# Optimization experiments

Measured on AMD Instinct MI355X. Metric: run time of the kernel, lower is better.

## Reference

```python
import jax, jax.numpy as jnp
import numpy as np

B, S, D = 1, 2048, 2048          # batch, context_length, embedding_dimension
H, DH = 16, 128                  # num_heads, head_size (= head_output_dimension)
HID = 4 * D                      # SwiGLU hidden dim
LAMBDA_INIT = 0.8
EPS = 1e-6


def setup_inputs() -> dict:
    key = jax.random.key(0)
    ks = jax.random.split(key, 14)
    nrm = lambda k, sh, s=0.02: jax.random.normal(k, sh, jnp.float32) * s
    return {
        "x": jax.random.normal(ks[0], (B, S, D), jnp.float32),
        "g_norm": jnp.ones((D,), jnp.float32),          # shared RMSNorm gain (same layer used twice)
        "Wq1": nrm(ks[1], (H, D, DH)), "Wq2": nrm(ks[2], (H, D, DH)),
        "Wk1": nrm(ks[3], (H, D, DH)), "Wk2": nrm(ks[4], (H, D, DH)),
        "Wv":  nrm(ks[5], (H, D, DH)),
        "lq1": nrm(ks[6], (H, DH), 0.1), "lk1": nrm(ks[7], (H, DH), 0.1),
        "lq2": nrm(ks[8], (H, DH), 0.1), "lk2": nrm(ks[9], (H, DH), 0.1),
        "Wo": nrm(ks[10], (H * DH, D)),
        "W1": nrm(ks[11], (D, HID)), "W2": nrm(ks[12], (D, HID)), "W3": nrm(ks[13], (HID, D)),
    }


def rmsnorm(x, g):
    return x * jax.lax.rsqrt(jnp.mean(x * x, axis=-1, keepdims=True) + EPS) * g


def diff_attention(x, Wq1, Wq2, Wk1, Wk2, Wv, lq1, lk1, lq2, lk2, Wo):
    # per-head projections: [B,S,D] x [H,D,DH] -> [B,H,S,DH]
    proj = lambda W: jnp.einsum('bsd,hde->bhse', x, W)
    q1, q2 = proj(Wq1), proj(Wq2)
    k1, k2 = proj(Wk1), proj(Wk2)
    v = proj(Wv)
    scale = 1.0 / jnp.sqrt(jnp.float32(DH))
    A1 = jax.nn.softmax(jnp.einsum('bhse,bhte->bhst', q1, k1) * scale, axis=-1)
    A2 = jax.nn.softmax(jnp.einsum('bhse,bhte->bhst', q2, k2) * scale, axis=-1)
    # learned per-head lambda: exp(lq1.lk1) - exp(lq2.lk2) + lambda_init
    lam = (jnp.exp(jnp.sum(lq1 * lk1, -1)) - jnp.exp(jnp.sum(lq2 * lk2, -1)) + LAMBDA_INIT)  # [H]
    o = jnp.einsum('bhst,bhte->bhse', A1 - lam[None, :, None, None] * A2, v)  # [B,H,S,DH]
    o = o.transpose(0, 2, 1, 3).reshape(B, S, H * DH)
    return o @ Wo


def reference(x, g_norm, Wq1, Wq2, Wk1, Wk2, Wv, lq1, lk1, lq2, lk2, Wo, W1, W2, W3):
    # Encoder block (dropout=0 -> identity in eval)
    h = rmsnorm(x, g_norm)
    h = diff_attention(h, Wq1, Wq2, Wk1, Wk2, Wv, lq1, lk1, lq2, lk2, Wo) + h
    z = rmsnorm(h, g_norm)
    ffn = (jax.nn.silu(z @ W1) * (z @ W2)) @ W3  # SwiGLU
    return ffn + h
```

## Files before the change

### kernel.cpp

```cpp
#include <hip/hip_runtime.h>

typedef unsigned short u16;
typedef __bf16 bf16x8 __attribute__((ext_vector_type(8)));
typedef float f32x4 __attribute__((ext_vector_type(4)));

#define S_LEN 2048
#define D_DIM 2048
#define NH 16
#define DH 128
#define HID 8192

__device__ __forceinline__ u16 f2bf(float f) {
  unsigned int u = __float_as_uint(f);
  u += 0x7fff + ((u >> 16) & 1);
  return (u16)(u >> 16);
}

__device__ __forceinline__ void gld16(const u16* g, u16* l) {
  __builtin_amdgcn_global_load_lds(
      (const __attribute__((address_space(1))) unsigned int*)g,
      (__attribute__((address_space(3))) unsigned int*)l, 16, 0, 0);
}

__global__ __launch_bounds__(256) void tconv_f2b(const float* __restrict__ in,
                                                 u16* __restrict__ out, int R, int C) {
  __shared__ float tile[32][33];
  size_t boff = (size_t)blockIdx.z * R * C;
  in += boff; out += boff;
  int c0 = blockIdx.x * 32, r0 = blockIdx.y * 32;
  int tx = threadIdx.x, ty = threadIdx.y;
#pragma unroll
  for (int i = 0; i < 32; i += 8) tile[ty + i][tx] = in[(size_t)(r0 + ty + i) * C + c0 + tx];
  __syncthreads();
#pragma unroll
  for (int i = 0; i < 32; i += 8) out[(size_t)(c0 + ty + i) * R + r0 + tx] = f2bf(tile[tx][ty + i]);
}

__global__ __launch_bounds__(256) void tconv_b2b(const u16* __restrict__ in,
                                                 u16* __restrict__ out, int R, int C) {
  __shared__ u16 tile[32][34];
  size_t boff = (size_t)blockIdx.z * R * C;
  in += boff; out += boff;
  int c0 = blockIdx.x * 32, r0 = blockIdx.y * 32;
  int tx = threadIdx.x, ty = threadIdx.y;
#pragma unroll
  for (int i = 0; i < 32; i += 8) tile[ty + i][tx] = in[(size_t)(r0 + ty + i) * C + c0 + tx];
  __syncthreads();
#pragma unroll
  for (int i = 0; i < 32; i += 8) out[(size_t)(c0 + ty + i) * R + r0 + tx] = tile[tx][ty + i];
}

__global__ __launch_bounds__(256) void rmsnorm_kernel(const float* __restrict__ x,
                                                      const float* __restrict__ g,
                                                      float* __restrict__ xf,
                                                      u16* __restrict__ xb) {
  int row = blockIdx.x;
  int t = threadIdx.x;
  const float4* xr = (const float4*)(x + (size_t)row * D_DIM);
  float4 v0 = xr[t];
  float4 v1 = xr[t + 256];
  float ss = v0.x * v0.x + v0.y * v0.y + v0.z * v0.z + v0.w * v0.w +
             v1.x * v1.x + v1.y * v1.y + v1.z * v1.z + v1.w * v1.w;
#pragma unroll
  for (int o = 1; o < 64; o <<= 1) ss += __shfl_xor(ss, o, 64);
  __shared__ float wss[4];
  if ((t & 63) == 0) wss[t >> 6] = ss;
  __syncthreads();
  float tot = wss[0] + wss[1] + wss[2] + wss[3];
  float rs = rsqrtf(tot * (1.0f / D_DIM) + 1e-6f);
  const float4* gr = (const float4*)g;
  float4 g0 = gr[t], g1 = gr[t + 256];
  float4 o0, o1;
  o0.x = v0.x * rs * g0.x; o0.y = v0.y * rs * g0.y; o0.z = v0.z * rs * g0.z; o0.w = v0.w * rs * g0.w;
  o1.x = v1.x * rs * g1.x; o1.y = v1.y * rs * g1.y; o1.z = v1.z * rs * g1.z; o1.w = v1.w * rs * g1.w;
  if (xf) {
    float4* xfr = (float4*)(xf + (size_t)row * D_DIM);
    xfr[t] = o0; xfr[t + 256] = o1;
  }
  ushort4 b0, b1;
  b0.x = f2bf(o0.x); b0.y = f2bf(o0.y); b0.z = f2bf(o0.z); b0.w = f2bf(o0.w);
  b1.x = f2bf(o1.x); b1.y = f2bf(o1.y); b1.z = f2bf(o1.z); b1.w = f2bf(o1.w);
  ushort4* xbr = (ushort4*)(xb + (size_t)row * D_DIM);
  xbr[t] = b0; xbr[t + 256] = b1;
}

__global__ __launch_bounds__(256) void lam_kernel(const float* __restrict__ lq1,
                                                  const float* __restrict__ lk1,
                                                  const float* __restrict__ lq2,
                                                  const float* __restrict__ lk2,
                                                  float* __restrict__ lamw) {
  int t = threadIdx.x;
  int h = t >> 4, i = (t & 15) << 3;
  float d1 = 0.f, d2 = 0.f;
#pragma unroll
  for (int j = 0; j < 8; j++) {
    d1 += lq1[h * DH + i + j] * lk1[h * DH + i + j];
    d2 += lq2[h * DH + i + j] * lk2[h * DH + i + j];
  }
#pragma unroll
  for (int o = 1; o < 16; o <<= 1) { d1 += __shfl_xor(d1, o, 64); d2 += __shfl_xor(d2, o, 64); }
  if ((t & 15) == 0) lamw[h] = __expf(d1) - __expf(d2) + 0.8f;
}

template <int MODE, int BN>
__global__ __launch_bounds__(256) void gemm_a(const u16* __restrict__ A,
                                              const u16* __restrict__ Bt,
                                              const u16* __restrict__ Bt2,
                                              void* __restrict__ Cout,
                                              const float* __restrict__ res,
                                              int M, int N, int K, long sBt, long sC) {
  constexpr int BM = 128, BK = 32;
  constexpr int JF = BN / 32;
  __shared__ __align__(16) u16 As[2][BM * BK];
  __shared__ __align__(16) u16 Bs[2][BN * BK];
  __shared__ __align__(16) u16 Bs2[(MODE == 2) ? 2 : 1][(MODE == 2) ? BN * BK : 8];
  const int t = threadIdx.x;
  const int lane = t & 63, wid = t >> 6;
  const int wm = (wid >> 1) * 64, wn = (wid & 1) * (BN / 2);
  const int fr = lane & 15, fq = lane >> 4;

  const int gx = gridDim.x, gy = gridDim.y;
  const int total = gx * gy * (int)gridDim.z;
  int flat = ((int)blockIdx.z * gy + (int)blockIdx.y) * gx + (int)blockIdx.x;
  {
    int q = total >> 3, r = total & 7;
    int xcd = flat & 7, pos = flat >> 3;
    flat = ((xcd < r) ? xcd * (q + 1) : r * (q + 1) + (xcd - r) * q) + pos;
  }
  const int bz = flat / (gx * gy);
  const int r2 = flat % (gx * gy);
  const int by = r2 / gx, bx = r2 % gx;

  const int m0 = by * BM, n0 = bx * BN;
  const u16* bt = Bt + (long)bz * sBt;
  f32x4 acc[4][JF] = {};
  f32x4 acc2[(MODE == 2) ? 4 : 1][(MODE == 2) ? JF : 1] = {};
  const int sr = t >> 2, sc = (t & 3) << 3;
  const u16* aG = A + (long)(m0 + sr) * K + sc;
  const u16* bG = bt + (long)(n0 + sr) * K + sc;
  const u16* b2G = (MODE == 2) ? (Bt2 + (long)(n0 + sr) * K + sc) : nullptr;

  auto stage = [&](int buf, int k0) {
    gld16(aG + k0, &As[buf][t * 8]);
    gld16(aG + (long)64 * K + k0, &As[buf][t * 8 + 64 * BK]);
    gld16(bG + k0, &Bs[buf][t * 8]);
    if (BN == 128) gld16(bG + (long)64 * K + k0, &Bs[buf][t * 8 + 64 * BK]);
    if (MODE == 2) {
      gld16(b2G + k0, &Bs2[buf][t * 8]);
      if (BN == 128) gld16(b2G + (long)64 * K + k0, &Bs2[buf][t * 8 + 64 * BK]);
    }
  };

  stage(0, 0);
  __syncthreads();

  int cur = 0;
  for (int k0 = 0; k0 < K; k0 += BK) {
    if (k0 + BK < K) stage(cur ^ 1, k0 + BK);

    bf16x8 af[4], bfr[JF];
#pragma unroll
    for (int i = 0; i < 4; i++) af[i] = *(const bf16x8*)&As[cur][(wm + i * 16 + fr) * BK + fq * 8];
#pragma unroll
    for (int j = 0; j < JF; j++) bfr[j] = *(const bf16x8*)&Bs[cur][(wn + j * 16 + fr) * BK + fq * 8];
    bf16x8 cf[(MODE == 2) ? JF : 1];
    if (MODE == 2) {
#pragma unroll
      for (int j = 0; j < JF; j++) cf[j] = *(const bf16x8*)&Bs2[cur][(wn + j * 16 + fr) * BK + fq * 8];
    }

    __builtin_amdgcn_s_setprio(1);
#pragma unroll
    for (int i = 0; i < 4; i++)
#pragma unroll
      for (int j = 0; j < JF; j++)
        acc[i][j] = __builtin_amdgcn_mfma_f32_16x16x32_bf16(af[i], bfr[j], acc[i][j], 0, 0, 0);
    if (MODE == 2) {
#pragma unroll
      for (int i = 0; i < 4; i++)
#pragma unroll
        for (int j = 0; j < JF; j++)
          acc2[i][j] = __builtin_amdgcn_mfma_f32_16x16x32_bf16(af[i], cf[j], acc2[i][j], 0, 0, 0);
    }
    __builtin_amdgcn_s_setprio(0);

    __syncthreads();
    cur ^= 1;
  }

#pragma unroll
  for (int i = 0; i < 4; i++)
#pragma unroll
    for (int j = 0; j < JF; j++) {
      int row0 = m0 + wm + i * 16 + (fq << 2);
      int col = n0 + wn + j * 16 + fr;
#pragma unroll
      for (int r = 0; r < 4; r++) {
        long idx = (long)(row0 + r) * N + col;
        float v = acc[i][j][r];
        if (MODE == 0) {
          ((u16*)Cout + (long)bz * sC)[idx] = f2bf(v);
        } else if (MODE == 1) {
          ((float*)Cout)[idx] = v + res[idx];
        } else {
          float g2 = acc2[i][j][r];
          float sg = v / (1.0f + __expf(-v));
          ((u16*)Cout)[idx] = f2bf(sg * g2);
        }
      }
    }
}

#define LDK 136
#define LDV 40
#define LDP 40

__global__ __launch_bounds__(256) void flash_attn(const u16* __restrict__ q1g,
                                                  const u16* __restrict__ q2g,
                                                  const u16* __restrict__ k1g,
                                                  const u16* __restrict__ k2g,
                                                  const u16* __restrict__ vtg,
                                                  const float* __restrict__ lamw,
                                                  u16* __restrict__ og) {
  __shared__ __align__(16) u16 Ks1[32 * LDK];
  __shared__ __align__(16) u16 Ks2[32 * LDK];
  __shared__ __align__(16) u16 Vs[128 * LDV];
  __shared__ __align__(16) u16 Ps[4 * 2 * 16 * LDP];
  const float scale = 0.08838834764831845f;
  int h = blockIdx.y, qt = blockIdx.x;
  size_t hoff = (size_t)h * S_LEN * DH;
  const u16* q1 = q1g + hoff;
  const u16* q2 = q2g + hoff;
  const u16* k1 = k1g + hoff;
  const u16* k2 = k2g + hoff;
  const u16* vt = vtg + hoff;
  int t = threadIdx.x, wid = t >> 6, lane = t & 63;
  int fr = lane & 15, fq = lane >> 4;
  int qrow = qt * 64 + wid * 16 + fr;
  bf16x8 qf1[4], qf2[4];
#pragma unroll
  for (int ks = 0; ks < 4; ks++) {
    qf1[ks] = *(const bf16x8*)&q1[(size_t)qrow * DH + ks * 32 + fq * 8];
    qf2[ks] = *(const bf16x8*)&q2[(size_t)qrow * DH + ks * 32 + fq * 8];
  }
  bf16x8 ones;
#pragma unroll
  for (int i = 0; i < 8; i++) ones[i] = (__bf16)1.0f;

  f32x4 O1[8] = {};
  f32x4 O2[8] = {};
  f32x4 L1 = {};
  f32x4 L2 = {};
  int skr = t >> 3, skc = (t & 7) << 4;
  int svr = t >> 2, svc = (t & 3) << 3;
  u16* myP1 = &Ps[(wid * 2 + 0) * 16 * LDP];
  u16* myP2 = &Ps[(wid * 2 + 1) * 16 * LDP];

  for (int kt = 0; kt < S_LEN; kt += 32) {
    uint4 ka1 = *(const uint4*)&k1[(size_t)(kt + skr) * DH + skc];
    uint4 kb1 = *(const uint4*)&k1[(size_t)(kt + skr) * DH + skc + 8];
    uint4 ka2 = *(const uint4*)&k2[(size_t)(kt + skr) * DH + skc];
    uint4 kb2 = *(const uint4*)&k2[(size_t)(kt + skr) * DH + skc + 8];
    uint4 va = *(const uint4*)&vt[(size_t)svr * S_LEN + kt + svc];
    uint4 vb = *(const uint4*)&vt[(size_t)(svr + 64) * S_LEN + kt + svc];
    __syncthreads();
    *(uint4*)&Ks1[skr * LDK + skc] = ka1;
    *(uint4*)&Ks1[skr * LDK + skc + 8] = kb1;
    *(uint4*)&Ks2[skr * LDK + skc] = ka2;
    *(uint4*)&Ks2[skr * LDK + skc + 8] = kb2;
    *(uint4*)&Vs[svr * LDV + svc] = va;
    *(uint4*)&Vs[(svr + 64) * LDV + svc] = vb;
    __syncthreads();

    f32x4 s1[2] = {};
    f32x4 s2[2] = {};
#pragma unroll
    for (int nf = 0; nf < 2; nf++)
#pragma unroll
      for (int ks = 0; ks < 4; ks++) {
        bf16x8 b1v = *(const bf16x8*)&Ks1[(nf * 16 + fr) * LDK + ks * 32 + fq * 8];
        s1[nf] = __builtin_amdgcn_mfma_f32_16x16x32_bf16(qf1[ks], b1v, s1[nf], 0, 0, 0);
        bf16x8 b2v = *(const bf16x8*)&Ks2[(nf * 16 + fr) * LDK + ks * 32 + fq * 8];
        s2[nf] = __builtin_amdgcn_mfma_f32_16x16x32_bf16(qf2[ks], b2v, s2[nf], 0, 0, 0);
      }

#pragma unroll
    for (int nf = 0; nf < 2; nf++)
#pragma unroll
      for (int r = 0; r < 4; r++) {
        myP1[(fq * 4 + r) * LDP + nf * 16 + fr] = f2bf(__expf(s1[nf][r] * scale));
        myP2[(fq * 4 + r) * LDP + nf * 16 + fr] = f2bf(__expf(s2[nf][r] * scale));
      }
    asm volatile("s_waitcnt lgkmcnt(0)" ::: "memory");
    bf16x8 pa1 = *(const bf16x8*)&myP1[fr * LDP + fq * 8];
    bf16x8 pa2 = *(const bf16x8*)&myP2[fr * LDP + fq * 8];
    L1 = __builtin_amdgcn_mfma_f32_16x16x32_bf16(pa1, ones, L1, 0, 0, 0);
    L2 = __builtin_amdgcn_mfma_f32_16x16x32_bf16(pa2, ones, L2, 0, 0, 0);
#pragma unroll
    for (int f = 0; f < 8; f++) {
      bf16x8 bv = *(const bf16x8*)&Vs[(f * 16 + fr) * LDV + fq * 8];
      O1[f] = __builtin_amdgcn_mfma_f32_16x16x32_bf16(pa1, bv, O1[f], 0, 0, 0);
      O2[f] = __builtin_amdgcn_mfma_f32_16x16x32_bf16(pa2, bv, O2[f], 0, 0, 0);
    }
  }

  float lam = lamw[h];
#pragma unroll
  for (int r = 0; r < 4; r++) {
    float i1 = 1.0f / L1[r], i2 = lam / L2[r];
#pragma unroll
    for (int f = 0; f < 8; f++) {
      float val = O1[f][r] * i1 - O2[f][r] * i2;
      og[(size_t)(qt * 64 + wid * 16 + fq * 4 + r) * (NH * DH) + h * DH + f * 16 + fr] =
          f2bf(val);
    }
  }
}

extern "C" void kernel_launch(void* const* d_in, const int* in_sizes, int n_in,
                              void* d_out, int out_size, void* d_ws, size_t ws_size,
                              hipStream_t stream) {
  const float* x = (const float*)d_in[0];
  const float* g = (const float*)d_in[1];
  const float* Wq1 = (const float*)d_in[2];
  const float* Wq2 = (const float*)d_in[3];
  const float* Wk1 = (const float*)d_in[4];
  const float* Wk2 = (const float*)d_in[5];
  const float* Wv = (const float*)d_in[6];
  const float* lq1 = (const float*)d_in[7];
  const float* lk1 = (const float*)d_in[8];
  const float* lq2 = (const float*)d_in[9];
  const float* lk2 = (const float*)d_in[10];
  const float* Wo = (const float*)d_in[11];
  const float* W1 = (const float*)d_in[12];
  const float* W2 = (const float*)d_in[13];
  const float* W3 = (const float*)d_in[14];

  char* ws = (char*)d_ws;
  size_t off = 0;
  auto alloc = [&](size_t b) {
    char* p = ws + off;
    off += (b + 255) & ~(size_t)255;
    return p;
  };
  const size_t PROJ_B = (size_t)NH * DH * D_DIM * 2;
  u16* wq1t = (u16*)alloc(PROJ_B);
  u16* wq2t = (u16*)alloc(PROJ_B);
  u16* wk1t = (u16*)alloc(PROJ_B);
  u16* wk2t = (u16*)alloc(PROJ_B);
  u16* wvt = (u16*)alloc(PROJ_B);
  u16* wot = (u16*)alloc((size_t)D_DIM * NH * DH * 2);
  u16* w1t = (u16*)alloc((size_t)HID * D_DIM * 2);
  u16* w2t = (u16*)alloc((size_t)HID * D_DIM * 2);
  u16* w3t = (u16*)alloc((size_t)D_DIM * HID * 2);
  u16* xnb = (u16*)alloc((size_t)S_LEN * D_DIM * 2);
  float* xnf = (float*)alloc((size_t)S_LEN * D_DIM * 4);
  u16* q1b = (u16*)alloc(PROJ_B);
  u16* q2b = (u16*)alloc(PROJ_B);
  u16* k1b = (u16*)alloc(PROJ_B);
  u16* k2b = (u16*)alloc(PROJ_B);
  u16* vb = (u16*)alloc(PROJ_B);
  u16* vtb = (u16*)alloc(PROJ_B);
  float* lamw = (float*)alloc(NH * 4);
  u16* oa = (u16*)alloc((size_t)S_LEN * NH * DH * 2);
  float* hf = (float*)alloc((size_t)S_LEN * D_DIM * 4);
  u16* zb = (u16*)alloc((size_t)S_LEN * D_DIM * 2);
  u16* ffb = (u16*)alloc((size_t)S_LEN * HID * 2);
  if (off > ws_size) return;

  dim3 tpb(32, 8);
  tconv_f2b<<<dim3(DH / 32, D_DIM / 32, NH), tpb, 0, stream>>>(Wq1, wq1t, D_DIM, DH);
  tconv_f2b<<<dim3(DH / 32, D_DIM / 32, NH), tpb, 0, stream>>>(Wq2, wq2t, D_DIM, DH);
  tconv_f2b<<<dim3(DH / 32, D_DIM / 32, NH), tpb, 0, stream>>>(Wk1, wk1t, D_DIM, DH);
  tconv_f2b<<<dim3(DH / 32, D_DIM / 32, NH), tpb, 0, stream>>>(Wk2, wk2t, D_DIM, NH == 16 ? DH : DH);
  tconv_f2b<<<dim3(DH / 32, D_DIM / 32, NH), tpb, 0, stream>>>(Wv, wvt, D_DIM, DH);
  tconv_f2b<<<dim3(D_DIM / 32, (NH * DH) / 32, 1), tpb, 0, stream>>>(Wo, wot, NH * DH, D_DIM);
  tconv_f2b<<<dim3(HID / 32, D_DIM / 32, 1), tpb, 0, stream>>>(W1, w1t, D_DIM, HID);
  tconv_f2b<<<dim3(HID / 32, D_DIM / 32, 1), tpb, 0, stream>>>(W2, w2t, D_DIM, HID);
  tconv_f2b<<<dim3(D_DIM / 32, HID / 32, 1), tpb, 0, stream>>>(W3, w3t, HID, D_DIM);

  rmsnorm_kernel<<<S_LEN, 256, 0, stream>>>(x, g, xnf, xnb);
  lam_kernel<<<1, 256, 0, stream>>>(lq1, lk1, lq2, lk2, lamw);

  long sB = (long)DH * D_DIM, sC = (long)S_LEN * DH;
  gemm_a<0, 128><<<dim3(1, S_LEN / 128, 80), 256, 0, stream>>>(
      xnb, wq1t, nullptr, q1b, nullptr, S_LEN, DH, D_DIM, sB, sC);
  tconv_b2b<<<dim3(DH / 32, S_LEN / 32, NH), tpb, 0, stream>>>(vb, vtb, S_LEN, DH);

  flash_attn<<<dim3(S_LEN / 64, NH), 256, 0, stream>>>(q1b, q2b, k1b, k2b, vtb, lamw, oa);

  gemm_a<1, 64><<<dim3(D_DIM / 64, S_LEN / 128, 1), 256, 0, stream>>>(
      oa, wot, nullptr, hf, xnf, S_LEN, D_DIM, NH * DH, 0, 0);
  rmsnorm_kernel<<<S_LEN, 256, 0, stream>>>(hf, g, nullptr, zb);
  gemm_a<2, 64><<<dim3(HID / 64, S_LEN / 128, 1), 256, 0, stream>>>(
      zb, w1t, w2t, ffb, nullptr, S_LEN, HID, D_DIM, 0, 0);
  gemm_a<1, 64><<<dim3(D_DIM / 64, S_LEN / 128, 1), 256, 0, stream>>>(
      ffb, w3t, nullptr, d_out, hf, S_LEN, D_DIM, HID, 0, 0);
}
```

Before: 978.9 us.

## Add dedicated 256x128 triple-buffered GEMM for fused QKV projections; drop XCD remap

Replaces the generic gemm_a launch for the five per-head projections with a new 512-thread kernel using 256x128x64 tiles, three-stage LDS buffering with XOR-swizzled layout, and interleaved prefetch with MFMA phases under raised priority. It treats all five projection weights as one N=10240 matrix, so outputs land in per-head layout. It also removes the XCD-aware block remapping from gemm_a, which may change L2 locality for the remaining GEMMs. The larger tile raises LDS use (about 144 KB) and register pressure, which limits occupancy.

After: 979.0 us. Within noise of the previous version (+0.0%).

```diff
diff --git a/kernel.cpp b/kernel.cpp
--- a/kernel.cpp
+++ b/kernel.cpp
@@ -100,6 +100,110 @@
 #pragma unroll
   for (int o = 1; o < 16; o <<= 1) { d1 += __shfl_xor(d1, o, 64); d2 += __shfl_xor(d2, o, 64); }
   if ((t & 15) == 0) lamw[h] = __expf(d1) - __expf(d2) + 0.8f;
+}
+
+__global__ __launch_bounds__(512) void gemm8_proj(const u16* __restrict__ A,
+                                                  const u16* __restrict__ Bt,
+                                                  u16* __restrict__ Out,
+                                                  int M, int N, int K) {
+  constexpr int BM = 256, BN = 128, BK = 64, NBUF = 3;
+  __shared__ __align__(16) u16 As[NBUF][BM * BK];
+  __shared__ __align__(16) u16 Bs[NBUF][BN * BK];
+  const int t = threadIdx.x;
+  const int lane = t & 63;
+  const int wid = t >> 6;
+  const int wm = (wid >> 2) * 128;
+  const int wn = (wid & 3) * 32;
+  const int fr = lane & 15, fq = lane >> 4;
+  const int m0 = blockIdx.y * BM, n0 = blockIdx.x * BN;
+
+  f32x4 acc[8][2] = {};
+
+  const int sro = t >> 3;
+  const int scol = ((((t & 7) ^ (sro & 7)) << 4) >> 1);
+  const u16* aSrc = A + (size_t)(m0 + sro) * K + scol;
+  const u16* bSrc = Bt + (size_t)(n0 + sro) * K + scol;
+
+  const int NT = K >> 6;
+
+#define STAGE_A(buf, k0, s) gld16(aSrc + (size_t)((s)*64) * K + (k0), &As[buf][(s)*4096 + t * 8])
+#define STAGE_B(buf, k0, s) gld16(bSrc + (size_t)((s)*64) * K + (k0), &Bs[buf][(s)*4096 + t * 8])
+
+  STAGE_A(0, 0, 0); STAGE_A(0, 0, 1); STAGE_A(0, 0, 2); STAGE_A(0, 0, 3);
+  STAGE_B(0, 0, 0); STAGE_B(0, 0, 1);
+  STAGE_A(1, BK, 0); STAGE_A(1, BK, 1); STAGE_A(1, BK, 2); STAGE_A(1, BK, 3);
+  STAGE_B(1, BK, 0); STAGE_B(1, BK, 1);
+  asm volatile("s_waitcnt vmcnt(6)" ::: "memory");
+  __builtin_amdgcn_s_barrier();
+
+  const int swz = (fr & 7) << 4;
+
+  for (int tk = 0; tk < NT; ++tk) {
+    const int r = tk % 3;
+    const int pf = tk + 2;
+    const int pbuf = pf % 3;
+    const bool doPf = pf < NT;
+    const int k0pf = pf << 6;
+
+    bf16x8 bfrag[2][2];
+#pragma unroll
+    for (int j = 0; j < 2; ++j)
+#pragma unroll
+      for (int kk = 0; kk < 2; ++kk) {
+        int row = wn + j * 16 + fr;
+        int cb = (kk * 64 + fq * 16) ^ swz;
+        bfrag[j][kk] = *(const bf16x8*)&Bs[r][row * 64 + (cb >> 1)];
+      }
+
+#pragma unroll
+    for (int ph = 0; ph < 2; ++ph) {
+      if (doPf) {
+        if (ph == 0) { STAGE_A(pbuf, k0pf, 0); STAGE_A(pbuf, k0pf, 1); STAGE_B(pbuf, k0pf, 0); }
+        else         { STAGE_A(pbuf, k0pf, 2); STAGE_A(pbuf, k0pf, 3); STAGE_B(pbuf, k0pf, 1); }
+      }
+      bf16x8 af[4][2];
+#pragma unroll
+      for (int i = 0; i < 4; ++i)
+#pragma unroll
+        for (int kk = 0; kk < 2; ++kk) {
+          int row = wm + ph * 64 + i * 16 + fr;
+          int cb = (kk * 64 + fq * 16) ^ swz;
+          af[i][kk] = *(const bf16x8*)&As[r][row * 64 + (cb >> 1)];
+        }
+      __builtin_amdgcn_s_setprio(1);
+#pragma unroll
+      for (int i = 0; i < 4; ++i)
+#pragma unroll
+        for (int j = 0; j < 2; ++j) {
+          acc[ph * 4 + i][j] =
+              __builtin_amdgcn_mfma_f32_16x16x32_bf16(af[i][0], bfrag[j][0], acc[ph * 4 + i][j], 0, 0, 0);
+          acc[ph * 4 + i][j] =
+              __builtin_amdgcn_mfma_f32_16x16x32_bf16(af[i][1], bfrag[j][1], acc[ph * 4 + i][j], 0, 0, 0);
+        }
+      __builtin_amdgcn_s_setprio(0);
+    }
+
+    if (tk + 1 < NT) {
+      if (doPf) asm volatile("s_waitcnt vmcnt(6)" ::: "memory");
+      else      asm volatile("s_waitcnt vmcnt(0)" ::: "memory");
+      __builtin_amdgcn_s_barrier();
+    }
+  }
+
+#undef STAGE_A
+#undef STAGE_B
+
+  const size_t headBase = (size_t)(n0 >> 7) * ((size_t)S_LEN * 128);
+#pragma unroll
+  for (int i = 0; i < 8; ++i)
+#pragma unroll
+    for (int j = 0; j < 2; ++j) {
+      int row0 = m0 + wm + i * 16 + (fq << 2);
+      int colL = wn + j * 16 + fr;
+#pragma unroll
+      for (int rr = 0; rr < 4; ++rr)
+        Out[headBase + (size_t)(row0 + rr) * 128 + colL] = f2bf(acc[i][j][rr]);
+    }
 }
 
 template <int MODE, int BN>
@@ -118,20 +222,8 @@
   const int lane = t & 63, wid = t >> 6;
   const int wm = (wid >> 1) * 64, wn = (wid & 1) * (BN / 2);
   const int fr = lane & 15, fq = lane >> 4;
-
-  const int gx = gridDim.x, gy = gridDim.y;
-  const int total = gx * gy * (int)gridDim.z;
-  int flat = ((int)blockIdx.z * gy + (int)blockIdx.y) * gx + (int)blockIdx.x;
-  {
-    int q = total >> 3, r = total & 7;
-    int xcd = flat & 7, pos = flat >> 3;
-    flat = ((xcd < r) ? xcd * (q + 1) : r * (q + 1) + (xcd - r) * q) + pos;
-  }
-  const int bz = flat / (gx * gy);
-  const int r2 = flat % (gx * gy);
-  const int by = r2 / gx, bx = r2 % gx;
-
-  const int m0 = by * BM, n0 = bx * BN;
+  const int m0 = blockIdx.y * BM, n0 = blockIdx.x * BN;
+  const int bz = blockIdx.z;
   const u16* bt = Bt + (long)bz * sBt;
   f32x4 acc[4][JF] = {};
   f32x4 acc2[(MODE == 2) ? 4 : 1][(MODE == 2) ? JF : 1] = {};
@@ -372,7 +464,7 @@
   tconv_f2b<<<dim3(DH / 32, D_DIM / 32, NH), tpb, 0, stream>>>(Wq1, wq1t, D_DIM, DH);
   tconv_f2b<<<dim3(DH / 32, D_DIM / 32, NH), tpb, 0, stream>>>(Wq2, wq2t, D_DIM, DH);
   tconv_f2b<<<dim3(DH / 32, D_DIM / 32, NH), tpb, 0, stream>>>(Wk1, wk1t, D_DIM, DH);
-  tconv_f2b<<<dim3(DH / 32, D_DIM / 32, NH), tpb, 0, stream>>>(Wk2, wk2t, D_DIM, NH == 16 ? DH : DH);
+  tconv_f2b<<<dim3(DH / 32, D_DIM / 32, NH), tpb, 0, stream>>>(Wk2, wk2t, D_DIM, DH);
   tconv_f2b<<<dim3(DH / 32, D_DIM / 32, NH), tpb, 0, stream>>>(Wv, wvt, D_DIM, DH);
   tconv_f2b<<<dim3(D_DIM / 32, (NH * DH) / 32, 1), tpb, 0, stream>>>(Wo, wot, NH * DH, D_DIM);
   tconv_f2b<<<dim3(HID / 32, D_DIM / 32, 1), tpb, 0, stream>>>(W1, w1t, D_DIM, HID);
@@ -382,9 +474,8 @@
   rmsnorm_kernel<<<S_LEN, 256, 0, stream>>>(x, g, xnf, xnb);
   lam_kernel<<<1, 256, 0, stream>>>(lq1, lk1, lq2, lk2, lamw);
 
-  long sB = (long)DH * D_DIM, sC = (long)S_LEN * DH;
-  gemm_a<0, 128><<<dim3(1, S_LEN / 128, 80), 256, 0, stream>>>(
-      xnb, wq1t, nullptr, q1b, nullptr, S_LEN, DH, D_DIM, sB, sC);
+  gemm8_proj<<<dim3((5 * NH * DH) / 128, S_LEN / 256), 512, 0, stream>>>(
+      xnb, wq1t, q1b, S_LEN, 5 * NH * DH, D_DIM);
   tconv_b2b<<<dim3(DH / 32, S_LEN / 32, NH), tpb, 0, stream>>>(vb, vtb, S_LEN, DH);
 
   flash_attn<<<dim3(S_LEN / 64, NH), 256, 0, stream>>>(q1b, q2b, k1b, k2b, vtb, lamw, oa);
```
